# Optimization experiments

Measured on AMD Instinct MI355X. Metric: run time of the kernel, lower is better.

The kernel has to match this reference:

```python
import jax, jax.numpy as jnp
import numpy as np

N_NODES = 50000
N_EDGES = 400000


def _gcn_norm(edge_index, num_nodes):
    """Add self-loops and compute symmetric GCN normalization coefficients.

    Returns (src, dst, norm) where out[dst] += norm * h[src].
    """
    loop = jnp.arange(num_nodes, dtype=edge_index.dtype)
    src = jnp.concatenate([edge_index[0], loop])
    dst = jnp.concatenate([edge_index[1], loop])
    ones = jnp.ones(src.shape[0], dtype=jnp.float32)
    deg = jax.ops.segment_sum(ones, dst, num_segments=num_nodes)
    d_inv_sqrt = jnp.where(deg > 0, jax.lax.rsqrt(jnp.maximum(deg, 1.0)), 0.0)
    norm = d_inv_sqrt[src] * d_inv_sqrt[dst]
    return src, dst, norm


def _gcn_conv(x, W, b, src, dst, norm, num_nodes):
    h = x @ W                              # [N, out] dense GEMM first (PyG GCNConv order)
    msg = h[src] * norm[:, None]           # [E+N, out] gather + scale
    agg = jax.ops.segment_sum(msg, dst, num_segments=num_nodes)  # scatter-add
    return agg + b


def setup_inputs() -> dict:
    key = jax.random.key(0)
    k1, k2, k3, k4, k5, k6 = jax.random.split(key, 6)
    x = jax.random.normal(k1, (N_NODES, 128), dtype=jnp.float32)
    edge_index = jax.random.randint(k2, (2, N_EDGES), 0, N_NODES, dtype=jnp.int64)
    # Glorot-ish scaled params
    W1 = jax.random.normal(k3, (128, 512), dtype=jnp.float32) * (1.0 / np.sqrt(128))
    b1 = jnp.zeros((512,), dtype=jnp.float32)
    W2 = jax.random.normal(k4, (512, 250), dtype=jnp.float32) * (1.0 / np.sqrt(512))
    b2 = jnp.zeros((250,), dtype=jnp.float32)
    return {"x": x, "edge_index": edge_index, "W1": W1, "b1": b1, "W2": W2, "b2": b2}


def reference(x, edge_index, W1, b1, W2, b2):
    num_nodes = x.shape[0]
    src, dst, norm = _gcn_norm(edge_index, num_nodes)
    h = _gcn_conv(x, W1, b1, src, dst, norm, num_nodes)
    h = jax.nn.relu(h)
    h = _gcn_conv(h, W2, b2, src, dst, norm, num_nodes)
    return jax.nn.relu(h)
```

## Files before the change

kernel.cpp:

```cpp
#include <hip/hip_runtime.h>

constexpr int NN  = 50000;
constexpr int NE  = 400000;
constexpr int F0  = 128;
constexpr int F1  = 512;
constexpr int F2  = 250;
constexpr int MT64 = 782;
constexpr int SLOT = 64;

typedef short  short8 __attribute__((ext_vector_type(8)));
typedef float  f32x4  __attribute__((ext_vector_type(4)));

__device__ inline unsigned short f2bf(float f) {
    union { float f; unsigned u; } v; v.f = f;
    unsigned u = v.u;
    return (unsigned short)((u + 0x7FFFu + ((u >> 16) & 1u)) >> 16);
}
__device__ inline float bf2f(unsigned short h) {
    union { unsigned u; float f; } v; v.u = ((unsigned)h) << 16;
    return v.f;
}
__device__ inline float bflo(unsigned u) {
    union { unsigned u; float f; } v; v.u = u << 16; return v.f;
}
__device__ inline float bfhi(unsigned u) {
    union { unsigned u; float f; } v; v.u = u & 0xFFFF0000u; return v.f;
}

__global__ void k_build(const int4* __restrict__ src4, const int4* __restrict__ dst4,
                        int* __restrict__ cnt, int* __restrict__ slot) {
    int t = blockIdx.x * 256 + threadIdx.x;
    if (t >= NE / 4) return;
    int4 s = src4[t];
    int4 d = dst4[t];
    int p;
    p = atomicAdd(&cnt[d.x], 1); if (p < SLOT) slot[d.x * SLOT + p] = s.x;
    p = atomicAdd(&cnt[d.y], 1); if (p < SLOT) slot[d.y * SLOT + p] = s.y;
    p = atomicAdd(&cnt[d.z], 1); if (p < SLOT) slot[d.z * SLOT + p] = s.z;
    p = atomicAdd(&cnt[d.w], 1); if (p < SLOT) slot[d.w * SLOT + p] = s.w;
}

__global__ __launch_bounds__(256) void k_prep(
        const float4* __restrict__ x4, const int* __restrict__ cnt,
        ushort4* __restrict__ xs,
        const float* __restrict__ W1, unsigned short* __restrict__ w1t,
        const float* __restrict__ W2, unsigned short* __restrict__ w2t) {
    int b = blockIdx.x;
    if (b < 6250) {
        int t = b * 256 + threadIdx.x;
        float dn = rsqrtf((float)cnt[t >> 5] + 1.0f);
        float4 v = x4[t];
        ushort4 o;
        o.x = f2bf(dn * v.x); o.y = f2bf(dn * v.y);
        o.z = f2bf(dn * v.z); o.w = f2bf(dn * v.w);
        xs[t] = o;
    } else if (b < 6250 + 256) {
        int t = (b - 6250) * 256 + threadIdx.x;
        int n = t >> 7, k = t & 127;
        w1t[t] = f2bf(W1[k * F1 + n]);
    } else {
        int t = (b - 6506) * 256 + threadIdx.x;
        int n = t >> 9, k = t & 511;
        w2t[t] = (n < F2) ? f2bf(W2[k * F2 + n]) : (unsigned short)0;
    }
}

__global__ __launch_bounds__(256) void k_fused1(
        const unsigned int* __restrict__ xs, const int* __restrict__ slot,
        const int* __restrict__ cnt, const unsigned short* __restrict__ Bt,
        const float* __restrict__ bias, unsigned short* __restrict__ C)
{
    __shared__ unsigned short As[64 * 128];
    __shared__ unsigned short Bs[128 * 128];
    unsigned int* As32 = (unsigned int*)As;

    const int tid = threadIdx.x;
    const int wv = tid >> 6, ln = tid & 63;
    const int m0 = blockIdx.x * 64;
    const int wy = wv >> 1, wx = wv & 1;
    const int lane15 = ln & 15, quad = ln >> 4;

    const int qch = ln >> 2;
    const int cu  = ln & 3;
    for (int i = 0; i < 16; ++i) {
        int m = wv * 16 + i;
        int n = m0 + m;
        int nc = n < NN ? n : NN - 1;
        int deg = cnt[nc]; if (deg > SLOT) deg = SLOT;
        float dn = rsqrtf((float)deg + 1.0f);
        const int* sl = slot + nc * SLOT;
        unsigned a = xs[(size_t)nc * 64 + ln];
        float s0 = bflo(a), s1 = bfhi(a);
        int j = 0;
        for (; j + 8 <= deg; j += 8) {
            int i0 = sl[j],     i1 = sl[j + 1], i2 = sl[j + 2], i3 = sl[j + 3];
            int i4 = sl[j + 4], i5 = sl[j + 5], i6 = sl[j + 6], i7 = sl[j + 7];
            unsigned v0 = xs[(size_t)i0 * 64 + ln];
            unsigned v1 = xs[(size_t)i1 * 64 + ln];
            unsigned v2 = xs[(size_t)i2 * 64 + ln];
            unsigned v3 = xs[(size_t)i3 * 64 + ln];
            unsigned v4 = xs[(size_t)i4 * 64 + ln];
            unsigned v5 = xs[(size_t)i5 * 64 + ln];
            unsigned v6 = xs[(size_t)i6 * 64 + ln];
            unsigned v7 = xs[(size_t)i7 * 64 + ln];
            s0 += bflo(v0) + bflo(v1) + bflo(v2) + bflo(v3)
                + bflo(v4) + bflo(v5) + bflo(v6) + bflo(v7);
            s1 += bfhi(v0) + bfhi(v1) + bfhi(v2) + bfhi(v3)
                + bfhi(v4) + bfhi(v5) + bfhi(v6) + bfhi(v7);
        }
        for (; j + 4 <= deg; j += 4) {
            int i0 = sl[j], i1 = sl[j + 1], i2 = sl[j + 2], i3 = sl[j + 3];
            unsigned v0 = xs[(size_t)i0 * 64 + ln];
            unsigned v1 = xs[(size_t)i1 * 64 + ln];
            unsigned v2 = xs[(size_t)i2 * 64 + ln];
            unsigned v3 = xs[(size_t)i3 * 64 + ln];
            s0 += bflo(v0) + bflo(v1) + bflo(v2) + bflo(v3);
            s1 += bfhi(v0) + bfhi(v1) + bfhi(v2) + bfhi(v3);
        }
        for (; j < deg; ++j) {
            unsigned v = xs[(size_t)sl[j] * 64 + ln];
            s0 += bflo(v); s1 += bfhi(v);
        }
        unsigned res = (n < NN)
            ? ((unsigned)f2bf(dn * s0) | ((unsigned)f2bf(dn * s1) << 16))
            : 0u;
        As32[m * 64 + ((qch ^ (m & 15)) << 2) + cu] = res;
    }
    __syncthreads();

    for (int nb = 0; nb < 4; ++nb) {
        const unsigned short* Bb = Bt + (size_t)nb * 128 * 128;
#pragma unroll
        for (int i = 0; i < 8; ++i) {
            int c = i * 256 + tid;
            int nr = c >> 4, q = c & 15;
            int gq = q ^ (nr & 15);
            __builtin_amdgcn_global_load_lds(
                (const __attribute__((address_space(1))) void*)(Bb + (size_t)nr * 128 + gq * 8),
                (__attribute__((address_space(3))) void*)(Bs + (i * 4 + wv) * 512), 16, 0, 0);
        }
        __syncthreads();

        f32x4 acc[2][4];
#pragma unroll
        for (int fy = 0; fy < 2; ++fy)
#pragma unroll
            for (int fx = 0; fx < 4; ++fx)
                acc[fy][fx] = (f32x4)0.0f;

#pragma unroll
        for (int kk = 0; kk < 4; ++kk) {
            short8 af[2], bf[4];
#pragma unroll
            for (int f = 0; f < 2; ++f) {
                int mA = wy * 32 + f * 16 + lane15;
                int sA = (kk * 4 + quad) ^ (mA & 15);
                af[f] = *(const short8*)(As + mA * 128 + sA * 8);
            }
#pragma unroll
            for (int f = 0; f < 4; ++f) {
                int nB = wx * 64 + f * 16 + lane15;
                int sB = (kk * 4 + quad) ^ (nB & 15);
                bf[f] = *(const short8*)(Bs + nB * 128 + sB * 8);
            }
#pragma unroll
            for (int fy = 0; fy < 2; ++fy)
#pragma unroll
                for (int fx = 0; fx < 4; ++fx)
                    acc[fy][fx] = __builtin_amdgcn_mfma_f32_16x16x32_bf16(
                        af[fy], bf[fx], acc[fy][fx], 0, 0, 0);
        }

#pragma unroll
        for (int fy = 0; fy < 2; ++fy) {
            int rowb = m0 + wy * 32 + fy * 16 + quad * 4;
#pragma unroll
            for (int fx = 0; fx < 4; ++fx) {
                int col = nb * 128 + wx * 64 + fx * 16 + lane15;
                float bia = bias[col];
                f32x4 v = acc[fy][fx];
#pragma unroll
                for (int r = 0; r < 4; ++r) {
                    int row = rowb + r;
                    if (row < NN)
                        C[(size_t)row * F1 + col] = f2bf(fmaxf(v[r] + bia, 0.0f));
                }
            }
        }
        if (nb < 3) __syncthreads();
    }
}

__global__ __launch_bounds__(256) void k_gemm_bf16(
        const unsigned short* __restrict__ A, int lda,
        const unsigned short* __restrict__ Bt, int ldb,
        unsigned short* __restrict__ C, int ldc,
        const int* __restrict__ cnt,
        int M, int K)
{
    __shared__ unsigned short As[2][64 * 32];
    __shared__ unsigned short Bs[2][128 * 32];

    const int tid = threadIdx.x;
    const int wv = tid >> 6, ln = tid & 63;
    const int m0 = blockIdx.y * 64, n0 = blockIdx.x * 128;
    const int wy = wv >> 1, wx = wv & 1;
    const int lane15 = ln & 15, quad = ln >> 4;

    const int cA = tid, mA_ = cA >> 2, qA = cA & 3;
    const int gqA = qA ^ ((mA_ >> 1) & 3);
    int arow = m0 + mA_; if (arow > M - 1) arow = M - 1;
    const unsigned short* agp = A + (size_t)arow * lda + gqA * 8;
    const int aofs = wv * 512;

    const unsigned short* bgp[2];
    int bofs[2];
#pragma unroll
    for (int i = 0; i < 2; ++i) {
        int c = (i * 4 + wv) * 64 + ln;
        int m = c >> 2, q = c & 3;
        int gq = q ^ ((m >> 1) & 3);
        bgp[i] = Bt + (size_t)(n0 + m) * ldb + gq * 8;
        bofs[i] = (i * 4 + wv) * 512;
    }

    f32x4 acc[2][4];
#pragma unroll
    for (int fy = 0; fy < 2; ++fy)
#pragma unroll
        for (int fx = 0; fx < 4; ++fx)
            acc[fy][fx] = (f32x4)0.0f;

    const int NK = K >> 5;

    __builtin_amdgcn_global_load_lds(
        (const __attribute__((address_space(1))) void*)agp,
        (__attribute__((address_space(3))) void*)(&As[0][0] + aofs), 16, 0, 0);
#pragma unroll
    for (int i = 0; i < 2; ++i)
        __builtin_amdgcn_global_load_lds(
            (const __attribute__((address_space(1))) void*)bgp[i],
            (__attribute__((address_space(3))) void*)(&Bs[0][0] + bofs[i]), 16, 0, 0);

    for (int ks = 0; ks < NK; ++ks) {
        __syncthreads();
        if (ks + 1 < NK) {
            int ko = (ks + 1) << 5;
            int nb = (ks + 1) & 1;
            __builtin_amdgcn_global_load_lds(
                (const __attribute__((address_space(1))) void*)(agp + ko),
                (__attribute__((address_space(3))) void*)(&As[nb][0] + aofs), 16, 0, 0);
#pragma unroll
            for (int i = 0; i < 2; ++i)
                __builtin_amdgcn_global_load_lds(
                    (const __attribute__((address_space(1))) void*)(bgp[i] + ko),
                    (__attribute__((address_space(3))) void*)(&Bs[nb][0] + bofs[i]), 16, 0, 0);
        }
        const int b = ks & 1;
        short8 af[2], bf[4];
#pragma unroll
        for (int f = 0; f < 2; ++f) {
            int mA = wy * 32 + f * 16 + lane15;
            int sA = quad ^ ((mA >> 1) & 3);
            af[f] = *(const short8*)(&As[b][0] + mA * 32 + sA * 8);
        }
#pragma unroll
        for (int f = 0; f < 4; ++f) {
            int nB = wx * 64 + f * 16 + lane15;
            int sB = quad ^ ((nB >> 1) & 3);
            bf[f] = *(const short8*)(&Bs[b][0] + nB * 32 + sB * 8);
        }
#pragma unroll
        for (int fy = 0; fy < 2; ++fy)
#pragma unroll
            for (int fx = 0; fx < 4; ++fx)
                acc[fy][fx] = __builtin_amdgcn_mfma_f32_16x16x32_bf16(
                    af[fy], bf[fx], acc[fy][fx], 0, 0, 0);
    }

#pragma unroll
    for (int fy = 0; fy < 2; ++fy) {
        int rowb = m0 + wy * 32 + fy * 16 + quad * 4;
        float rs[4];
#pragma unroll
        for (int r = 0; r < 4; ++r) {
            int row = rowb + r; if (row > M - 1) row = M - 1;
            rs[r] = rsqrtf((float)cnt[row] + 1.0f);
        }
#pragma unroll
        for (int fx = 0; fx < 4; ++fx) {
            int col = n0 + wx * 64 + fx * 16 + lane15;
            f32x4 v = acc[fy][fx];
#pragma unroll
            for (int r = 0; r < 4; ++r) {
                int row = rowb + r;
                if (row < M)
                    C[(size_t)row * ldc + col] = f2bf(v[r] * rs[r]);
            }
        }
    }
}

__global__ __launch_bounds__(256) void k_gather2(
        const ushort4* __restrict__ t4, const int* __restrict__ slot,
        const int* __restrict__ cnt, const float* __restrict__ b2,
        float* __restrict__ out) {
    int n = blockIdx.x * 4 + (threadIdx.x >> 6);
    int c = threadIdx.x & 63;
    if (n >= NN) return;
    int deg = cnt[n]; if (deg > SLOT) deg = SLOT;
    float dn = rsqrtf((float)deg + 1.0f);
    const int* sl = slot + n * SLOT;
    ushort4 a = t4[(size_t)n * 64 + c];
    float sx = bf2f(a.x), sy = bf2f(a.y), sz = bf2f(a.z), sw = bf2f(a.w);
    int j = 0;
    for (; j + 8 <= deg; j += 8) {
        int i0 = sl[j],     i1 = sl[j + 1], i2 = sl[j + 2], i3 = sl[j + 3];
        int i4 = sl[j + 4], i5 = sl[j + 5], i6 = sl[j + 6], i7 = sl[j + 7];
        ushort4 v0 = t4[(size_t)i0 * 64 + c];
        ushort4 v1 = t4[(size_t)i1 * 64 + c];
        ushort4 v2 = t4[(size_t)i2 * 64 + c];
        ushort4 v3 = t4[(size_t)i3 * 64 + c];
        ushort4 v4 = t4[(size_t)i4 * 64 + c];
        ushort4 v5 = t4[(size_t)i5 * 64 + c];
        ushort4 v6 = t4[(size_t)i6 * 64 + c];
        ushort4 v7 = t4[(size_t)i7 * 64 + c];
        sx += bf2f(v0.x) + bf2f(v1.x) + bf2f(v2.x) + bf2f(v3.x)
            + bf2f(v4.x) + bf2f(v5.x) + bf2f(v6.x) + bf2f(v7.x);
        sy += bf2f(v0.y) + bf2f(v1.y) + bf2f(v2.y) + bf2f(v3.y)
            + bf2f(v4.y) + bf2f(v5.y) + bf2f(v6.y) + bf2f(v7.y);
        sz += bf2f(v0.z) + bf2f(v1.z) + bf2f(v2.z) + bf2f(v3.z)
            + bf2f(v4.z) + bf2f(v5.z) + bf2f(v6.z) + bf2f(v7.z);
        sw += bf2f(v0.w) + bf2f(v1.w) + bf2f(v2.w) + bf2f(v3.w)
            + bf2f(v4.w) + bf2f(v5.w) + bf2f(v6.w) + bf2f(v7.w);
    }
    for (; j + 4 <= deg; j += 4) {
        int i0 = sl[j], i1 = sl[j + 1], i2 = sl[j + 2], i3 = sl[j + 3];
        ushort4 v0 = t4[(size_t)i0 * 64 + c];
        ushort4 v1 = t4[(size_t)i1 * 64 + c];
        ushort4 v2 = t4[(size_t)i2 * 64 + c];
        ushort4 v3 = t4[(size_t)i3 * 64 + c];
        sx += bf2f(v0.x) + bf2f(v1.x) + bf2f(v2.x) + bf2f(v3.x);
        sy += bf2f(v0.y) + bf2f(v1.y) + bf2f(v2.y) + bf2f(v3.y);
        sz += bf2f(v0.z) + bf2f(v1.z) + bf2f(v2.z) + bf2f(v3.z);
        sw += bf2f(v0.w) + bf2f(v1.w) + bf2f(v2.w) + bf2f(v3.w);
    }
    for (; j < deg; ++j) {
        ushort4 v = t4[(size_t)sl[j] * 64 + c];
        sx += bf2f(v.x); sy += bf2f(v.y); sz += bf2f(v.z); sw += bf2f(v.w);
    }
    int f = c * 4;
    float* o = out + (size_t)n * F2;
    if (f     < F2) o[f]     = fmaxf(dn * sx + b2[f],     0.f);
    if (f + 1 < F2) o[f + 1] = fmaxf(dn * sy + b2[f + 1], 0.f);
    if (f + 2 < F2) o[f + 2] = fmaxf(dn * sz + b2[f + 2], 0.f);
    if (f + 3 < F2) o[f + 3] = fmaxf(dn * sw + b2[f + 3], 0.f);
}

extern "C" void kernel_launch(void* const* d_in, const int* in_sizes, int n_in,
                              void* d_out, int out_size, void* d_ws, size_t ws_size,
                              hipStream_t stream) {
    const float* x  = (const float*)d_in[0];
    const int*   ei = (const int*)d_in[1];
    const float* W1 = (const float*)d_in[2];
    const float* b1 = (const float*)d_in[3];
    const float* W2 = (const float*)d_in[4];
    const float* b2 = (const float*)d_in[5];
    float* out = (float*)d_out;

    char* p = (char*)d_ws;
    auto carve = [&](size_t bytes) { char* r = p; p += (bytes + 255) & ~(size_t)255; return r; };
    int*            cnt  = (int*)carve(NN * 4);
    int*            slot = (int*)carve((size_t)NN * SLOT * 4);
    unsigned short* xs   = (unsigned short*)carve((size_t)NN * F0 * 2);
    unsigned short* h1   = (unsigned short*)carve((size_t)NN * F1 * 2);
    unsigned short* t2s  = (unsigned short*)carve((size_t)NN * 256 * 2);
    unsigned short* w1t  = (unsigned short*)carve((size_t)F1 * F0 * 2);
    unsigned short* w2t  = (unsigned short*)carve((size_t)256 * F1 * 2);

    hipMemsetAsync(cnt, 0, NN * sizeof(int), stream);
    k_build<<<(NE / 4 + 255) / 256, 256, 0, stream>>>(
        (const int4*)ei, (const int4*)(ei + NE), cnt, slot);
    k_prep<<<6250 + 256 + 512, 256, 0, stream>>>(
        (const float4*)x, cnt, (ushort4*)xs, W1, w1t, W2, w2t);
    k_fused1<<<MT64, 256, 0, stream>>>((const unsigned int*)xs, slot, cnt, w1t, b1, h1);
    k_gemm_bf16<<<dim3(256 / 128, MT64), 256, 0, stream>>>(
        h1, F1, w2t, F1, t2s, 256, cnt, NN, F1);
    k_gather2<<<(NN + 3) / 4, 256, 0, stream>>>((const ushort4*)t2s, slot, cnt, b2, out);
}
```

Before: 281.2 us.

## Split fused gather+GEMM1 into separate kernels and widen GEMM2 tile to 256 cols

```diff
diff --git a/kernel.cpp b/kernel.cpp
--- a/kernel.cpp
+++ b/kernel.cpp
@@ -65,14 +65,144 @@
     }
 }
 
-__global__ __launch_bounds__(256) void k_fused1(
+__global__ __launch_bounds__(256) void k_gather1(
         const unsigned int* __restrict__ xs, const int* __restrict__ slot,
-        const int* __restrict__ cnt, const unsigned short* __restrict__ Bt,
-        const float* __restrict__ bias, unsigned short* __restrict__ C)
+        const int* __restrict__ cnt, unsigned int* __restrict__ agg) {
+    int n = blockIdx.x * 4 + (threadIdx.x >> 6);
+    int c = threadIdx.x & 63;
+    if (n >= NN) return;
+    int deg = cnt[n]; if (deg > SLOT) deg = SLOT;
+    float dn = rsqrtf((float)deg + 1.0f);
+    const int* sl = slot + n * SLOT;
+    unsigned a = xs[(size_t)n * 64 + c];
+    float s0 = bflo(a), s1 = bfhi(a);
+    int j = 0;
+    for (; j + 8 <= deg; j += 8) {
+        int i0 = sl[j],     i1 = sl[j + 1], i2 = sl[j + 2], i3 = sl[j + 3];
+        int i4 = sl[j + 4], i5 = sl[j + 5], i6 = sl[j + 6], i7 = sl[j + 7];
+        unsigned v0 = xs[(size_t)i0 * 64 + c];
+        unsigned v1 = xs[(size_t)i1 * 64 + c];
+        unsigned v2 = xs[(size_t)i2 * 64 + c];
+        unsigned v3 = xs[(size_t)i3 * 64 + c];
+        unsigned v4 = xs[(size_t)i4 * 64 + c];
+        unsigned v5 = xs[(size_t)i5 * 64 + c];
+        unsigned v6 = xs[(size_t)i6 * 64 + c];
+        unsigned v7 = xs[(size_t)i7 * 64 + c];
+        s0 += bflo(v0) + bflo(v1) + bflo(v2) + bflo(v3)
+            + bflo(v4) + bflo(v5) + bflo(v6) + bflo(v7);
+        s1 += bfhi(v0) + bfhi(v1) + bfhi(v2) + bfhi(v3)
+            + bfhi(v4) + bfhi(v5) + bfhi(v6) + bfhi(v7);
+    }
+    for (; j + 4 <= deg; j += 4) {
+        int i0 = sl[j], i1 = sl[j + 1], i2 = sl[j + 2], i3 = sl[j + 3];
+        unsigned v0 = xs[(size_t)i0 * 64 + c];
+        unsigned v1 = xs[(size_t)i1 * 64 + c];
+        unsigned v2 = xs[(size_t)i2 * 64 + c];
+        unsigned v3 = xs[(size_t)i3 * 64 + c];
+        s0 += bflo(v0) + bflo(v1) + bflo(v2) + bflo(v3);
+        s1 += bfhi(v0) + bfhi(v1) + bfhi(v2) + bfhi(v3);
+    }
+    for (; j < deg; ++j) {
+        unsigned v = xs[(size_t)sl[j] * 64 + c];
+        s0 += bflo(v); s1 += bfhi(v);
+    }
+    agg[(size_t)n * 64 + c] =
+        (unsigned)f2bf(dn * s0) | ((unsigned)f2bf(dn * s1) << 16);
+}
+
+__global__ __launch_bounds__(256) void k_gemm1(
+        const unsigned short* __restrict__ A,
+        const unsigned short* __restrict__ Bt,
+        unsigned short* __restrict__ C,
+        const float* __restrict__ bias, int M)
 {
     __shared__ unsigned short As[64 * 128];
     __shared__ unsigned short Bs[128 * 128];
-    unsigned int* As32 = (unsigned int*)As;
+
+    const int tid = threadIdx.x;
+    const int wv = tid >> 6, ln = tid & 63;
+    const int m0 = blockIdx.y * 64, n0 = blockIdx.x * 128;
+    const int wy = wv >> 1, wx = wv & 1;
+    const int lane15 = ln & 15, quad = ln >> 4;
+
+#pragma unroll
+    for (int i = 0; i < 4; ++i) {
+        int c = i * 256 + tid;
+        int m = c >> 4, q = c & 15;
+        int gq = q ^ (m & 15);
+        int arow = m0 + m; if (arow > M - 1) arow = M - 1;
+        __builtin_amdgcn_global_load_lds(
+            (const __attribute__((address_space(1))) void*)(A + (size_t)arow * 128 + gq * 8),
+            (__attribute__((address_space(3))) void*)(As + (i * 4 + wv) * 512), 16, 0, 0);
+    }
+#pragma unroll
+    for (int i = 0; i < 8; ++i) {
+        int c = i * 256 + tid;
+        int n = c >> 4, q = c & 15;
+        int gq = q ^ (n & 15);
+        __builtin_amdgcn_global_load_lds(
+            (const __attribute__((address_space(1))) void*)(Bt + (size_t)(n0 + n) * 128 + gq * 8),
+            (__attribute__((address_space(3))) void*)(Bs + (i * 4 + wv) * 512), 16, 0, 0);
+    }
+
+    f32x4 acc[2][4];
+#pragma unroll
+    for (int fy = 0; fy < 2; ++fy)
+#pragma unroll
+        for (int fx = 0; fx < 4; ++fx)
+            acc[fy][fx] = (f32x4)0.0f;
+
+    __syncthreads();
+
+#pragma unroll
+    for (int kk = 0; kk < 4; ++kk) {
+        short8 af[2], bf[4];
+#pragma unroll
+        for (int f = 0; f < 2; ++f) {
+            int mA = wy * 32 + f * 16 + lane15;
+            int sA = (kk * 4 + quad) ^ (mA & 15);
+            af[f] = *(const short8*)(As + mA * 128 + sA * 8);
+        }
+#pragma unroll
+        for (int f = 0; f < 4; ++f) {
+            int nB = wx * 64 + f * 16 + lane15;
+            int sB = (kk * 4 + quad) ^ (nB & 15);
+            bf[f] = *(const short8*)(Bs + nB * 128 + sB * 8);
+        }
+#pragma unroll
+        for (int fy = 0; fy < 2; ++fy)
+#pragma unroll
+            for (int fx = 0; fx < 4; ++fx)
+                acc[fy][fx] = __builtin_amdgcn_mfma_f32_16x16x32_bf16(
+                    af[fy], bf[fx], acc[fy][fx], 0, 0, 0);
+    }
+
+#pragma unroll
+    for (int fy = 0; fy < 2; ++fy) {
+        int rowb = m0 + wy * 32 + fy * 16 + quad * 4;
+#pragma unroll
+        for (int fx = 0; fx < 4; ++fx) {
+            int col = n0 + wx * 64 + fx * 16 + lane15;
+            float bia = bias[col];
+            f32x4 v = acc[fy][fx];
+#pragma unroll
+            for (int r = 0; r < 4; ++r) {
+                int row = rowb + r;
+                if (row < M)
+                    C[(size_t)row * F1 + col] = f2bf(fmaxf(v[r] + bia, 0.0f));
+            }
+        }
+    }
+}
+
+__global__ __launch_bounds__(256) void k_gemm2(
+        const unsigned short* __restrict__ A,
+        const unsigned short* __restrict__ Bt,
+        unsigned short* __restrict__ C,
+        const int* __restrict__ cnt, int M)
+{
+    __shared__ unsigned short As[2][64 * 32];
+    __shared__ unsigned short Bs[2][256 * 32];
 
     const int tid = threadIdx.x;
     const int wv = tid >> 6, ln = tid & 63;
@@ -80,164 +210,37 @@
     const int wy = wv >> 1, wx = wv & 1;
     const int lane15 = ln & 15, quad = ln >> 4;
 
-    const int qch = ln >> 2;
-    const int cu  = ln & 3;
-    for (int i = 0; i < 16; ++i) {
-        int m = wv * 16 + i;
-        int n = m0 + m;
-        int nc = n < NN ? n : NN - 1;
-        int deg = cnt[nc]; if (deg > SLOT) deg = SLOT;
-        float dn = rsqrtf((float)deg + 1.0f);
-        const int* sl = slot + nc * SLOT;
-        unsigned a = xs[(size_t)nc * 64 + ln];
-        float s0 = bflo(a), s1 = bfhi(a);
-        int j = 0;
-        for (; j + 8 <= deg; j += 8) {
-            int i0 = sl[j],     i1 = sl[j + 1], i2 = sl[j + 2], i3 = sl[j + 3];
-            int i4 = sl[j + 4], i5 = sl[j + 5], i6 = sl[j + 6], i7 = sl[j + 7];
-            unsigned v0 = xs[(size_t)i0 * 64 + ln];
-            unsigned v1 = xs[(size_t)i1 * 64 + ln];
-            unsigned v2 = xs[(size_t)i2 * 64 + ln];
-            unsigned v3 = xs[(size_t)i3 * 64 + ln];
-            unsigned v4 = xs[(size_t)i4 * 64 + ln];
-            unsigned v5 = xs[(size_t)i5 * 64 + ln];
-            unsigned v6 = xs[(size_t)i6 * 64 + ln];
-            unsigned v7 = xs[(size_t)i7 * 64 + ln];
-            s0 += bflo(v0) + bflo(v1) + bflo(v2) + bflo(v3)
-                + bflo(v4) + bflo(v5) + bflo(v6) + bflo(v7);
-            s1 += bfhi(v0) + bfhi(v1) + bfhi(v2) + bfhi(v3)
-                + bfhi(v4) + bfhi(v5) + bfhi(v6) + bfhi(v7);
-        }
-        for (; j + 4 <= deg; j += 4) {
-            int i0 = sl[j], i1 = sl[j + 1], i2 = sl[j + 2], i3 = sl[j + 3];
-            unsigned v0 = xs[(size_t)i0 * 64 + ln];
-            unsigned v1 = xs[(size_t)i1 * 64 + ln];
-            unsigned v2 = xs[(size_t)i2 * 64 + ln];
-            unsigned v3 = xs[(size_t)i3 * 64 + ln];
-            s0 += bflo(v0) + bflo(v1) + bflo(v2) + bflo(v3);
-            s1 += bfhi(v0) + bfhi(v1) + bfhi(v2) + bfhi(v3);
-        }
-        for (; j < deg; ++j) {
-            unsigned v = xs[(size_t)sl[j] * 64 + ln];
-            s0 += bflo(v); s1 += bfhi(v);
-        }
-        unsigned res = (n < NN)
-            ? ((unsigned)f2bf(dn * s0) | ((unsigned)f2bf(dn * s1) << 16))
-            : 0u;
-        As32[m * 64 + ((qch ^ (m & 15)) << 2) + cu] = res;
-    }
-    __syncthreads();
-
-    for (int nb = 0; nb < 4; ++nb) {
-        const unsigned short* Bb = Bt + (size_t)nb * 128 * 128;
-#pragma unroll
-        for (int i = 0; i < 8; ++i) {
-            int c = i * 256 + tid;
-            int nr = c >> 4, q = c & 15;
-            int gq = q ^ (nr & 15);
-            __builtin_amdgcn_global_load_lds(
-                (const __attribute__((address_space(1))) void*)(Bb + (size_t)nr * 128 + gq * 8),
-                (__attribute__((address_space(3))) void*)(Bs + (i * 4 + wv) * 512), 16, 0, 0);
-        }
-        __syncthreads();
-
-        f32x4 acc[2][4];
-#pragma unroll
-        for (int fy = 0; fy < 2; ++fy)
-#pragma unroll
-            for (int fx = 0; fx < 4; ++fx)
-                acc[fy][fx] = (f32x4)0.0f;
-
-#pragma unroll
-        for (int kk = 0; kk < 4; ++kk) {
-            short8 af[2], bf[4];
-#pragma unroll
-            for (int f = 0; f < 2; ++f) {
-                int mA = wy * 32 + f * 16 + lane15;
-                int sA = (kk * 4 + quad) ^ (mA & 15);
-                af[f] = *(const short8*)(As + mA * 128 + sA * 8);
-            }
-#pragma unroll
-            for (int f = 0; f < 4; ++f) {
-                int nB = wx * 64 + f * 16 + lane15;
-                int sB = (kk * 4 + quad) ^ (nB & 15);
-                bf[f] = *(const short8*)(Bs + nB * 128 + sB * 8);
-            }
-#pragma unroll
-            for (int fy = 0; fy < 2; ++fy)
-#pragma unroll
-                for (int fx = 0; fx < 4; ++fx)
-                    acc[fy][fx] = __builtin_amdgcn_mfma_f32_16x16x32_bf16(
-                        af[fy], bf[fx], acc[fy][fx], 0, 0, 0);
-        }
-
-#pragma unroll
-        for (int fy = 0; fy < 2; ++fy) {
-            int rowb = m0 + wy * 32 + fy * 16 + quad * 4;
-#pragma unroll
-            for (int fx = 0; fx < 4; ++fx) {
-                int col = nb * 128 + wx * 64 + fx * 16 + lane15;
-                float bia = bias[col];
-                f32x4 v = acc[fy][fx];
-#pragma unroll
-                for (int r = 0; r < 4; ++r) {
-                    int row = rowb + r;
-                    if (row < NN)
-                        C[(size_t)row * F1 + col] = f2bf(fmaxf(v[r] + bia, 0.0f));
-                }
-            }
-        }
-        if (nb < 3) __syncthreads();
-    }
-}
-
-__global__ __launch_bounds__(256) void k_gemm_bf16(
-        const unsigned short* __restrict__ A, int lda,
-        const unsigned short* __restrict__ Bt, int ldb,
-        unsigned short* __restrict__ C, int ldc,
-        const int* __restrict__ cnt,
-        int M, int K)
-{
-    __shared__ unsigned short As[2][64 * 32];
-    __shared__ unsigned short Bs[2][128 * 32];
-
-    const int tid = threadIdx.x;
-    const int wv = tid >> 6, ln = tid & 63;
-    const int m0 = blockIdx.y * 64, n0 = blockIdx.x * 128;
-    const int wy = wv >> 1, wx = wv & 1;
-    const int lane15 = ln & 15, quad = ln >> 4;
-
-    const int cA = tid, mA_ = cA >> 2, qA = cA & 3;
+    const int mA_ = tid >> 2, qA = tid & 3;
     const int gqA = qA ^ ((mA_ >> 1) & 3);
     int arow = m0 + mA_; if (arow > M - 1) arow = M - 1;
-    const unsigned short* agp = A + (size_t)arow * lda + gqA * 8;
+    const unsigned short* agp = A + (size_t)arow * F1 + gqA * 8;
     const int aofs = wv * 512;
 
-    const unsigned short* bgp[2];
-    int bofs[2];
-#pragma unroll
-    for (int i = 0; i < 2; ++i) {
+    const unsigned short* bgp[4];
+    int bofs[4];
+#pragma unroll
+    for (int i = 0; i < 4; ++i) {
         int c = (i * 4 + wv) * 64 + ln;
-        int m = c >> 2, q = c & 3;
-        int gq = q ^ ((m >> 1) & 3);
-        bgp[i] = Bt + (size_t)(n0 + m) * ldb + gq * 8;
+        int n = c >> 2, q = c & 3;
+        int gq = q ^ ((n >> 1) & 3);
+        bgp[i] = Bt + (size_t)n * F1 + gq * 8;
         bofs[i] = (i * 4 + wv) * 512;
     }
 
-    f32x4 acc[2][4];
+    f32x4 acc[2][8];
 #pragma unroll
     for (int fy = 0; fy < 2; ++fy)
 #pragma unroll
-        for (int fx = 0; fx < 4; ++fx)
+        for (int fx = 0; fx < 8; ++fx)
             acc[fy][fx] = (f32x4)0.0f;
 
-    const int NK = K >> 5;
+    const int NK = F1 / 32;
 
     __builtin_amdgcn_global_load_lds(
         (const __attribute__((address_space(1))) void*)agp,
         (__attribute__((address_space(3))) void*)(&As[0][0] + aofs), 16, 0, 0);
 #pragma unroll
-    for (int i = 0; i < 2; ++i)
+    for (int i = 0; i < 4; ++i)
         __builtin_amdgcn_global_load_lds(
             (const __attribute__((address_space(1))) void*)bgp[i],
             (__attribute__((address_space(3))) void*)(&Bs[0][0] + bofs[i]), 16, 0, 0);
@@ -251,13 +254,13 @@
                 (const __attribute__((address_space(1))) void*)(agp + ko),
                 (__attribute__((address_space(3))) void*)(&As[nb][0] + aofs), 16, 0, 0);
 #pragma unroll
-            for (int i = 0; i < 2; ++i)
+            for (int i = 0; i < 4; ++i)
                 __builtin_amdgcn_global_load_lds(
                     (const __attribute__((address_space(1))) void*)(bgp[i] + ko),
                     (__attribute__((address_space(3))) void*)(&Bs[nb][0] + bofs[i]), 16, 0, 0);
         }
         const int b = ks & 1;
-        short8 af[2], bf[4];
+        short8 af[2], bf[8];
 #pragma unroll
         for (int f = 0; f < 2; ++f) {
             int mA = wy * 32 + f * 16 + lane15;
@@ -265,15 +268,15 @@
             af[f] = *(const short8*)(&As[b][0] + mA * 32 + sA * 8);
         }
 #pragma unroll
-        for (int f = 0; f < 4; ++f) {
-            int nB = wx * 64 + f * 16 + lane15;
+        for (int f = 0; f < 8; ++f) {
+            int nB = wx * 128 + f * 16 + lane15;
             int sB = quad ^ ((nB >> 1) & 3);
             bf[f] = *(const short8*)(&Bs[b][0] + nB * 32 + sB * 8);
         }
 #pragma unroll
         for (int fy = 0; fy < 2; ++fy)
 #pragma unroll
-            for (int fx = 0; fx < 4; ++fx)
+            for (int fx = 0; fx < 8; ++fx)
                 acc[fy][fx] = __builtin_amdgcn_mfma_f32_16x16x32_bf16(
                     af[fy], bf[fx], acc[fy][fx], 0, 0, 0);
     }
@@ -288,14 +291,14 @@
             rs[r] = rsqrtf((float)cnt[row] + 1.0f);
         }
 #pragma unroll
-        for (int fx = 0; fx < 4; ++fx) {
-            int col = n0 + wx * 64 + fx * 16 + lane15;
+        for (int fx = 0; fx < 8; ++fx) {
+            int col = wx * 128 + fx * 16 + lane15;
             f32x4 v = acc[fy][fx];
 #pragma unroll
             for (int r = 0; r < 4; ++r) {
                 int row = rowb + r;
                 if (row < M)
-                    C[(size_t)row * ldc + col] = f2bf(v[r] * rs[r]);
+                    C[(size_t)row * 256 + col] = f2bf(v[r] * rs[r]);
             }
         }
     }
@@ -373,6 +376,7 @@
     int*            cnt  = (int*)carve(NN * 4);
     int*            slot = (int*)carve((size_t)NN * SLOT * 4);
     unsigned short* xs   = (unsigned short*)carve((size_t)NN * F0 * 2);
+    unsigned short* agg1 = (unsigned short*)carve((size_t)NN * F0 * 2);
     unsigned short* h1   = (unsigned short*)carve((size_t)NN * F1 * 2);
     unsigned short* t2s  = (unsigned short*)carve((size_t)NN * 256 * 2);
     unsigned short* w1t  = (unsigned short*)carve((size_t)F1 * F0 * 2);
@@ -383,8 +387,9 @@
         (const int4*)ei, (const int4*)(ei + NE), cnt, slot);
     k_prep<<<6250 + 256 + 512, 256, 0, stream>>>(
         (const float4*)x, cnt, (ushort4*)xs, W1, w1t, W2, w2t);
-    k_fused1<<<MT64, 256, 0, stream>>>((const unsigned int*)xs, slot, cnt, w1t, b1, h1);
-    k_gemm_bf16<<<dim3(256 / 128, MT64), 256, 0, stream>>>(
-        h1, F1, w2t, F1, t2s, 256, cnt, NN, F1);
+    k_gather1<<<(NN + 3) / 4, 256, 0, stream>>>((const unsigned int*)xs, slot, cnt,
+                                                (unsigned int*)agg1);
+    k_gemm1<<<dim3(F1 / 128, MT64), 256, 0, stream>>>(agg1, w1t, h1, b1, NN);
+    k_gemm2<<<MT64, 256, 0, stream>>>(h1, w2t, t2s, cnt, NN);
     k_gather2<<<(NN + 3) / 4, 256, 0, stream>>>((const ushort4*)t2s, slot, cnt, b2, out);
 }
```

Result: faster. 238.7 us (-15.1%).
